# Performance work log

Hardware: AMD Instinct MI355X
Metric: run time of the kernel (lower is better)

The kernel has to match this reference:

```python
import jax, jax.numpy as jnp
import numpy as np


def setup_inputs() -> dict:
    key = jax.random.key(0)
    kx, kd = jax.random.split(key)
    B, S, D = 32, 1024, 384
    x = jax.random.normal(kx, (B, S, D), dtype=jnp.float32)
    durations = jax.random.randint(kd, (B, S), 0, 8, dtype=jnp.int64)
    return {"x": x, "durations": durations}


def reference(x, durations):
    # x: [B, S, D] float; durations: [B, S] int (frames per input step)
    B, S, D = x.shape
    out_lens = jnp.sum(durations, axis=1)            # [B]
    # max_len is data-dependent; materialize it concretely (eager / host-side)
    max_len = int(np.asarray(out_lens).max())
    cum = jnp.cumsum(durations, axis=1)              # [B, S] exclusive ends
    pos = jnp.arange(max_len)                        # [L]
    # For output position j, source index t = first t with cum[t] > j
    # (frame t occupies output slots [cum[t-1], cum[t])). This reproduces
    # torch repeat-interleave expansion, skipping zero-duration steps.
    idx = jax.vmap(lambda c: jnp.searchsorted(c, pos, side="right"))(cum)  # [B, L]
    idx = jnp.clip(idx, 0, S - 1)
    out = jnp.take_along_axis(x, idx[..., None], axis=1)  # [B, L, D]
    # Zero the padded tail (original writes into a zero-initialized buffer)
    valid = (pos[None, :] < out_lens[:, None])[..., None]  # [B, L, 1]
    out = jnp.where(valid, out, jnp.zeros((), dtype=x.dtype))
    return out, out_lens
```

## Files before the change

### kernel.cpp

```cpp
#include <hip/hip_runtime.h>
#include <hip/hip_bf16.h>


#define LR_B 32
#define LR_S 1024
#define LR_D 384
#define LR_V4 (LR_D / 4)

typedef float f32x4 __attribute__((ext_vector_type(4)));

__global__ __launch_bounds__(LR_S) void lr_build_idx_kernel(
    const int* __restrict__ dur, int* __restrict__ idx,
    float* __restrict__ out_tail, int L) {
  __shared__ int wsum[LR_S / 64];
  const int b = blockIdx.x;
  const int t = threadIdx.x;
  const int wave = t >> 6;
  const int lane = t & 63;
  const int d = dur[b * LR_S + t];

  int v = d;
#pragma unroll
  for (int off = 1; off < 64; off <<= 1) {
    int n = __shfl_up(v, off, 64);
    if (lane >= off) v += n;
  }
  if (lane == 63) wsum[wave] = v;
  __syncthreads();

  int woff = 0, tot = 0;
#pragma unroll
  for (int w = 0; w < LR_S / 64; ++w) {
    int s = wsum[w];
    if (w < wave) woff += s;
    tot += s;
  }
  const int end = woff + v;
  const int start = end - d;

  int* __restrict__ ib = idx + (size_t)b * L;
  const int src = b * LR_S + t;
  for (int j = start; j < end; ++j) ib[j] = src;
  for (int j = tot + t; j < L; j += LR_S) ib[j] = -1;

  if (t == 0) out_tail[b] = (float)tot;
}

__global__ __launch_bounds__(256) void lr_gather_kernel(
    const f32x4* __restrict__ x4, const int* __restrict__ idx,
    f32x4* __restrict__ out4, int total_v4) {
  const int gid = blockIdx.x * 256 + threadIdx.x;
  if (gid >= total_v4) return;
  const int row = gid / LR_V4;
  const int v = gid - row * LR_V4;
  const int src = idx[row];
  f32x4 val;
  if (src < 0) {
    val = (f32x4){0.f, 0.f, 0.f, 0.f};
  } else {
    val = x4[(size_t)src * LR_V4 + v];
  }
  __builtin_nontemporal_store(val, &out4[gid]);
}

extern "C" void kernel_launch(void* const* d_in, const int* in_sizes, int n_in,
                              void* d_out, int out_size, void* d_ws, size_t ws_size,
                              hipStream_t stream) {
  const float* x = (const float*)d_in[0];
  const int* dur = (const int*)d_in[1];
  float* out = (float*)d_out;

  const int L = (out_size - LR_B) / (LR_B * LR_D);

  int* idx = (int*)d_ws;
  float* out_tail = out + (size_t)LR_B * L * LR_D;

  lr_build_idx_kernel<<<LR_B, LR_S, 0, stream>>>(dur, idx, out_tail, L);

  const int total_v4 = LR_B * L * LR_V4;
  const int grid = (total_v4 + 255) / 256;
  lr_gather_kernel<<<grid, 256, 0, stream>>>(
      (const f32x4*)x, idx, (f32x4*)out, total_v4);
}
```

Measured before the change: 48.32 us.

## Fuse index build into gather kernel with per-block redundant prefix scan

```diff
diff --git a/kernel.cpp b/kernel.cpp
--- a/kernel.cpp
+++ b/kernel.cpp
@@ -6,61 +6,66 @@
 #define LR_S 1024
 #define LR_D 384
 #define LR_V4 (LR_D / 4)
+#define ROWS_PB 32
 
 typedef float f32x4 __attribute__((ext_vector_type(4)));
 
-__global__ __launch_bounds__(LR_S) void lr_build_idx_kernel(
-    const int* __restrict__ dur, int* __restrict__ idx,
-    float* __restrict__ out_tail, int L) {
-  __shared__ int wsum[LR_S / 64];
-  const int b = blockIdx.x;
+__global__ __launch_bounds__(256) void lr_fused_kernel(
+    const f32x4* __restrict__ x4, const int* __restrict__ dur,
+    f32x4* __restrict__ out4, float* __restrict__ out_tail, int L) {
+  __shared__ int wsum[4];
+  __shared__ int lidx[ROWS_PB];
+  const int b = blockIdx.y;
+  const int r0 = blockIdx.x * ROWS_PB;
   const int t = threadIdx.x;
-  const int wave = t >> 6;
-  const int lane = t & 63;
-  const int d = dur[b * LR_S + t];
+  const int wave = t >> 6, lane = t & 63;
 
-  int v = d;
+  const int4 d4 = ((const int4*)(dur + b * LR_S))[t];
+  const int e0 = d4.x, e1 = e0 + d4.y, e2 = e1 + d4.z, e3 = e2 + d4.w;
+  int v = e3;
 #pragma unroll
   for (int off = 1; off < 64; off <<= 1) {
     int n = __shfl_up(v, off, 64);
     if (lane >= off) v += n;
   }
   if (lane == 63) wsum[wave] = v;
+  if (t < ROWS_PB) lidx[t] = -1;
   __syncthreads();
 
   int woff = 0, tot = 0;
 #pragma unroll
-  for (int w = 0; w < LR_S / 64; ++w) {
+  for (int w = 0; w < 4; ++w) {
     int s = wsum[w];
     if (w < wave) woff += s;
     tot += s;
   }
-  const int end = woff + v;
-  const int start = end - d;
+  const int base = woff + v - e3;
 
-  int* __restrict__ ib = idx + (size_t)b * L;
-  const int src = b * LR_S + t;
-  for (int j = start; j < end; ++j) ib[j] = src;
-  for (int j = tot + t; j < L; j += LR_S) ib[j] = -1;
+  const int r1 = min(r0 + ROWS_PB, L);
+  const int starts[4] = {base, base + e0, base + e1, base + e2};
+  const int ends[4]   = {base + e0, base + e1, base + e2, base + e3};
+#pragma unroll
+  for (int k = 0; k < 4; ++k) {
+    const int s = max(starts[k], r0), e = min(ends[k], r1);
+    for (int j = s; j < e; ++j) lidx[j - r0] = t * 4 + k;
+  }
+  __syncthreads();
 
-  if (t == 0) out_tail[b] = (float)tot;
-}
+  const size_t obase = ((size_t)b * L + r0) * LR_V4;
+  const size_t xbase = (size_t)b * LR_S * LR_V4;
+#pragma unroll
+  for (int i = 0; i < ROWS_PB * LR_V4 / 256; ++i) {
+    const int p = i * 256 + t;
+    const int r = p / LR_V4;
+    const int vv = p - r * LR_V4;
+    if (r0 + r >= L) continue;
+    const int st = lidx[r];
+    f32x4 val = (st < 0) ? (f32x4){0.f, 0.f, 0.f, 0.f}
+                         : x4[xbase + (size_t)st * LR_V4 + vv];
+    __builtin_nontemporal_store(val, &out4[obase + p]);
+  }
 
-__global__ __launch_bounds__(256) void lr_gather_kernel(
-    const f32x4* __restrict__ x4, const int* __restrict__ idx,
-    f32x4* __restrict__ out4, int total_v4) {
-  const int gid = blockIdx.x * 256 + threadIdx.x;
-  if (gid >= total_v4) return;
-  const int row = gid / LR_V4;
-  const int v = gid - row * LR_V4;
-  const int src = idx[row];
-  f32x4 val;
-  if (src < 0) {
-    val = (f32x4){0.f, 0.f, 0.f, 0.f};
-  } else {
-    val = x4[(size_t)src * LR_V4 + v];
-  }
-  __builtin_nontemporal_store(val, &out4[gid]);
+  if (blockIdx.x == 0 && t == 0) out_tail[b] = (float)tot;
 }
 
 extern "C" void kernel_launch(void* const* d_in, const int* in_sizes, int n_in,
@@ -71,14 +76,10 @@
   float* out = (float*)d_out;
 
   const int L = (out_size - LR_B) / (LR_B * LR_D);
-
-  int* idx = (int*)d_ws;
   float* out_tail = out + (size_t)LR_B * L * LR_D;
 
-  lr_build_idx_kernel<<<LR_B, LR_S, 0, stream>>>(dur, idx, out_tail, L);
-
-  const int total_v4 = LR_B * L * LR_V4;
-  const int grid = (total_v4 + 255) / 256;
-  lr_gather_kernel<<<grid, 256, 0, stream>>>(
-      (const f32x4*)x, idx, (f32x4*)out, total_v4);
+  const int nchunks = (L + ROWS_PB - 1) / ROWS_PB;
+  dim3 grid(nchunks, LR_B);
+  lr_fused_kernel<<<grid, 256, 0, stream>>>(
+      (const f32x4*)x, dur, (f32x4*)out, out_tail, L);
 }
```

New measurement: 40.78 us, median of 2. 15.6% less time.
